# Kernel optimization log

Hardware: AMD Instinct MI355X
Metric: run time of the kernel (lower is better)

The kernel has to match this reference:

```python
import jax, jax.numpy as jnp
import numpy as np
from jax import lax

B, T, IN, H, DIM = 128, 1024, 64, 128, 64


def setup_inputs() -> dict:
    key = jax.random.key(0)
    ks = jax.random.split(key, 14)
    s = 0.05
    return {
        "x": jax.random.normal(ks[0], (B, T, IN), jnp.float32),
        "is_init": jax.random.randint(ks[1], (B, T, 1), 0, 2).astype(bool),
        "hx": jax.random.normal(ks[2], (B, H), jnp.float32),
        # MLP: Linear(IN,128) + ELU, Linear(128,128) + ELU
        "W1": jax.random.normal(ks[3], (128, IN), jnp.float32) * s,
        "b1": jnp.zeros((128,), jnp.float32),
        "W2": jax.random.normal(ks[4], (128, 128), jnp.float32) * s,
        "b2": jnp.zeros((128,), jnp.float32),
        # GRU params (torch layout: [3H, in] with gate order r,z,n)
        "W_ih": jax.random.normal(ks[5], (3 * H, 128), jnp.float32) * s,
        "b_ih": jnp.zeros((3 * H,), jnp.float32),
        "W_hh": jax.random.normal(ks[6], (3 * H, H), jnp.float32) * s,
        "b_hh": jnp.zeros((3 * H,), jnp.float32),
        # output head Linear(128, DIM)
        "W_out": jax.random.normal(ks[7], (DIM, 128), jnp.float32) * s,
        "b_out": jnp.zeros((DIM,), jnp.float32),
    }


def _gru_with_reset(xg, init_mask, h0, W_hh, b_hh):
    # xg: [T,B,3H] precomputed input-side gates; init_mask: [T,B,1] float
    def step(h, inp):
        xg_t, m_t = inp
        h = h * (1.0 - m_t)                       # reset hidden where is_init
        hg = h @ W_hh.T + b_hh                    # [B,3H]
        xr, xz, xn = jnp.split(xg_t, 3, axis=-1)
        hr, hz, hn = jnp.split(hg, 3, axis=-1)
        r = jax.nn.sigmoid(xr + hr)
        z = jax.nn.sigmoid(xz + hz)
        n = jnp.tanh(xn + r * hn)
        h_new = (1.0 - z) * n + z * h
        return h_new, h_new

    hT, ys = lax.scan(step, h0, (xg, init_mask))
    return ys, hT


def reference(x, is_init, hx, W1, b1, W2, b2, W_ih, b_ih, W_hh, b_hh, W_out, b_out):
    # MLP (ELU activations)
    h = jax.nn.elu(x @ W1.T + b1)
    h = jax.nn.elu(h @ W2.T + b2)                 # [B,T,128]
    # precompute input-side gate projections for all timesteps (one big GEMM)
    xg = h @ W_ih.T + b_ih                        # [B,T,3H]
    xg_t = jnp.transpose(xg, (1, 0, 2))           # [T,B,3H]
    m_t = jnp.transpose(is_init.astype(x.dtype), (1, 0, 2))  # [T,B,1]
    ys, hT = _gru_with_reset(xg_t, m_t, hx, W_hh, b_hh)
    y = jnp.transpose(ys, (1, 0, 2))              # [B,T,H]
    out = y @ W_out.T + b_out                     # [B,T,DIM]
    return out, hT
```

## Files before the change

kernel.cpp:

```cpp
#include <hip/hip_runtime.h>


#define T_SZ 1024

typedef __attribute__((ext_vector_type(8))) short short8;
typedef __attribute__((ext_vector_type(4))) float f32x4;
typedef unsigned long long u64;
typedef unsigned int uint32;

__device__ __forceinline__ unsigned short f2b(float f){
  return __builtin_bit_cast(unsigned short, (__bf16)f);
}
__device__ __forceinline__ float b2f(unsigned int hs){
  unsigned int u = hs << 16;
  return __builtin_bit_cast(float, u);
}
__device__ __forceinline__ short8 load_w8(const float* __restrict__ p){
  const float4* q = (const float4*)p;
  float4 u0 = q[0], u1 = q[1];
  short8 v;
  v[0]=(short)f2b(u0.x); v[1]=(short)f2b(u0.y); v[2]=(short)f2b(u0.z); v[3]=(short)f2b(u0.w);
  v[4]=(short)f2b(u1.x); v[5]=(short)f2b(u1.y); v[6]=(short)f2b(u1.z); v[7]=(short)f2b(u1.w);
  return v;
}
__device__ __forceinline__ float elu(float v){ return v > 0.f ? v : __expf(v) - 1.f; }
__device__ __forceinline__ float sigm(float x){ return 1.f / (1.f + __expf(-x)); }
__device__ __forceinline__ float tanh_fast(float x){
  x = fminf(fmaxf(x, -15.f), 15.f);
  float e = __expf(-2.f * x);
  return (1.f - e) / (1.f + e);
}
#define MFMA16(a,b,c) __builtin_amdgcn_mfma_f32_16x16x32_bf16(a, b, c, 0, 0, 0)


__global__ __launch_bounds__(512) void wprep(const float* __restrict__ Whh, uint4* __restrict__ wbf){
  int rec = blockIdx.x*512 + threadIdx.x;
  if(rec >= 6144) return;
  int q  = rec & 3;
  int n_ = (rec >> 2) & 127;
  int ks = (rec >> 9) & 3;
  int gt = rec >> 11;
  const float* p = Whh + (size_t)(n_ + 128*gt)*128 + ks*32 + q*8;
  uint4 o;
  o.x = (uint32)f2b(p[0]) | ((uint32)f2b(p[1]) << 16);
  o.y = (uint32)f2b(p[2]) | ((uint32)f2b(p[3]) << 16);
  o.z = (uint32)f2b(p[4]) | ((uint32)f2b(p[5]) << 16);
  o.w = (uint32)f2b(p[6]) | ((uint32)f2b(p[7]) << 16);
  wbf[rec] = o;
}

__global__ __launch_bounds__(512) void seg_build(const int* __restrict__ ii, uint32* C){
  __shared__ uint32 lh[1024];
  __shared__ uint32 lbase[1024];
  __shared__ uint32 ssum[512];
  __shared__ uint32 sbase;
  uint32* segs = C + 4096;
  const int tid = threadIdx.x;
  const int wv = tid >> 6, lane = tid & 63;
  const int b = blockIdx.x*8 + wv;

  for(int i = tid; i < 1024; i += 512) lh[i] = 0u;
  __syncthreads();

  u64 bal[16], mb[16];
  #pragma unroll
  for(int c=0;c<16;c++){
    int t = c*64 + lane;
    int m = ii[b*T_SZ + t];
    mb[c]  = __ballot(m != 0);
    bal[c] = __ballot((m != 0) || (t == 0));
  }
  int fsA[16]; int nx = T_SZ;
  #pragma unroll
  for(int c=15;c>=0;c--){ fsA[c]=nx; if(bal[c]) nx = c*64 + __builtin_ctzll(bal[c]); }

  int lenA[16], tA[16], rkA[16];
  #pragma unroll
  for(int c=0;c<16;c++){
    lenA[c] = 0;
    if((bal[c] >> lane) & 1ull){
      int t = c*64 + lane;
      u64 hi = (lane < 63) ? (bal[c] >> (lane+1)) : 0ull;
      int nxt = hi ? (t + 1 + __builtin_ctzll(hi)) : fsA[c];
      int len = nxt - t;
      int rst = (int)((mb[c] >> lane) & 1ull);
      len -= rst; t += rst;
      if(len > 0){
        lenA[c] = len; tA[c] = t;
        rkA[c] = (int)atomicAdd(&lh[1024 - len], 1u);
      }
    }
  }
  __syncthreads();

  uint32 c0 = lh[2*tid], c1 = lh[2*tid+1];
  ssum[tid] = c0 + c1;
  __syncthreads();
  #pragma unroll
  for(int off=1; off<512; off<<=1){
    uint32 v = (tid >= off) ? ssum[tid-off] : 0u;
    __syncthreads();
    ssum[tid] += v;
    __syncthreads();
  }
  uint32 excl = tid ? ssum[tid-1] : 0u;
  lbase[2*tid]   = excl;
  lbase[2*tid+1] = excl + c0;
  uint32 total = ssum[511];
  uint32 padded = (total + 15u) & ~15u;
  if(tid == 0){
    sbase = atomicAdd(&C[2], padded);
    atomicAdd(&C[1], padded >> 4);
  }
  __syncthreads();
  const uint32 base = sbase;

  #pragma unroll
  for(int c=0;c<16;c++){
    if(lenA[c] > 0){
      uint32 slot = base + lbase[1024 - lenA[c]] + (uint32)rkA[c];
      segs[slot] = ((uint32)b << 21) | ((uint32)tA[c] << 11) | (uint32)lenA[c];
    }
  }
  for(uint32 i = total + tid; i < padded; i += 512) segs[base + i] = 0u;
}

__global__ __launch_bounds__(512) void fused_mlp(
    const float* __restrict__ x, const int* __restrict__ ii,
    const float* __restrict__ W1, const float* __restrict__ b1,
    const float* __restrict__ W2, const float* __restrict__ b2,
    const float* __restrict__ Wih, const float* __restrict__ bih,
    const float* __restrict__ bhh,
    unsigned short* __restrict__ xg, unsigned short* __restrict__ ys,
    float* __restrict__ hT)
{
  __shared__ __align__(16) char smem[35840];
  unsigned short* xs  = (unsigned short*)smem;
  unsigned short* h1l = (unsigned short*)(smem + 18432);
  unsigned short* h2l = (unsigned short*)smem;
  __shared__ int iil[64];
  const int tid = threadIdx.x;
  const int wv = tid >> 6, l = tid & 63, quad = l >> 4, col = l & 15;
  const int n = 16*wv + col;

  short8 w1f[2], w2f[4], wif[3][4];
  #pragma unroll
  for(int ks=0; ks<2; ks++) w1f[ks] = load_w8(W1 + n*64  + ks*32 + quad*8);
  #pragma unroll
  for(int ks=0; ks<4; ks++) w2f[ks] = load_w8(W2 + n*128 + ks*32 + quad*8);
  #pragma unroll
  for(int gt=0; gt<3; gt++){
    #pragma unroll
    for(int ks=0; ks<4; ks++)
      wif[gt][ks] = load_w8(Wih + (n + 128*gt)*128 + ks*32 + quad*8);
  }
  const float b1v = b1[n], b2v = b2[n];
  float bihv[3], bhhv[3];
  #pragma unroll
  for(int gt=0; gt<3; gt++){ bihv[gt] = bih[n + 128*gt]; bhhv[gt] = bhh[n + 128*gt]; }

  const int srow = tid >> 5, sk = tid & 31;

  for(int tile = blockIdx.x; tile < 2048; tile += gridDim.x){
    const int g = tile & 7, t0 = (tile >> 3) * 4;
    __syncthreads();
    {
      const float* src = x + (size_t)(16*g + srow)*(T_SZ*64) + (size_t)t0*64;
      #pragma unroll
      for(int j=0; j<2; j++){
        int s = sk + 32*j;
        float4 v = ((const float4*)src)[s];
        int tt = s >> 4, k = (s & 15) * 4;
        unsigned short* dst = xs + (tt*16 + srow)*72 + k;
        dst[0]=f2b(v.x); dst[1]=f2b(v.y); dst[2]=f2b(v.z); dst[3]=f2b(v.w);
      }
    }
    if(tid < 64) iil[tid] = ii[(16*g + (tid & 15))*T_SZ + t0 + (tid >> 4)];
    __syncthreads();
    #pragma unroll
    for(int tt=0; tt<4; tt++){
      f32x4 acc = {b1v, b1v, b1v, b1v};
      #pragma unroll
      for(int ks=0; ks<2; ks++){
        short8 a = *(const short8*)&xs[(tt*16 + col)*72 + ks*32 + quad*8];
        acc = MFMA16(a, w1f[ks], acc);
      }
      #pragma unroll
      for(int r=0; r<4; r++)
        h1l[(tt*16 + quad*4 + r)*136 + n] = f2b(elu(acc[r]));
    }
    __syncthreads();
    #pragma unroll
    for(int tt=0; tt<4; tt++){
      f32x4 acc = {b2v, b2v, b2v, b2v};
      #pragma unroll
      for(int ks=0; ks<4; ks++){
        short8 a = *(const short8*)&h1l[(tt*16 + col)*136 + ks*32 + quad*8];
        acc = MFMA16(a, w2f[ks], acc);
      }
      #pragma unroll
      for(int r=0; r<4; r++)
        h2l[(tt*16 + quad*4 + r)*136 + n] = f2b(elu(acc[r]));
    }
    __syncthreads();
    uint32 xgo[4];
    #pragma unroll
    for(int r=0; r<4; r++)
      xgo[r] = (((uint32)(16*g + quad*4 + r) << 10) + (uint32)t0) * 384u + (uint32)n;
    #pragma unroll
    for(int tt=0; tt<4; tt++){
      f32x4 a0 = {bihv[0], bihv[0], bihv[0], bihv[0]};
      f32x4 a1 = {bihv[1], bihv[1], bihv[1], bihv[1]};
      f32x4 a2 = {bihv[2], bihv[2], bihv[2], bihv[2]};
      #pragma unroll
      for(int ks=0; ks<4; ks++){
        short8 a = *(const short8*)&h2l[(tt*16 + col)*136 + ks*32 + quad*8];
        a0 = MFMA16(a, wif[0][ks], a0);
        a1 = MFMA16(a, wif[1][ks], a1);
        a2 = MFMA16(a, wif[2][ks], a2);
      }
      const int t = t0 + tt;
      #pragma unroll
      for(int r=0; r<4; r++){
        int row = quad*4 + r;
        unsigned short* p = xg + xgo[r] + (uint32)(tt*384);
        p[0]   = f2b(a0[r]);
        p[128] = f2b(a1[r]);
        p[256] = f2b(a2[r]);
        if(iil[tt*16 + row] != 0){
          float rr = sigm(a0[r] + bhhv[0]);
          float zz = sigm(a1[r] + bhhv[1]);
          float nn = tanh_fast(a2[r] + rr*bhhv[2]);
          float h1 = (1.f - zz)*nn;
          ys[((size_t)(t*8 + g)*16 + row)*128 + n] = f2b(h1);
          if(t == T_SZ-1)
            hT[(16*g + row)*128 + n] = h1;
        }
      }
    }
  }
}

__global__ __launch_bounds__(512) void gru_seg_scan(
    const unsigned short* __restrict__ xg,
    const float* __restrict__ hx,
    const uint4* __restrict__ wbf, const float* __restrict__ bhh,
    const uint32* __restrict__ C,
    unsigned short* __restrict__ ys, float* __restrict__ hT)
{
  __shared__ unsigned short hl[2][16*136];
  __shared__ unsigned short xbuf[2][16*772];
  __shared__ int srb[16], srt[16], srlen[16];
  const uint32 ntile = C[1];
  const uint32 tile = blockIdx.x;
  if(tile >= ntile) return;

  const int tid = threadIdx.x;
  const int wv = tid >> 6, l = tid & 63, quad = l >> 4, col = l & 15;
  const int nidx = 16*wv + col;
  const int frow = tid >> 5, fk = tid & 31;
  const uint32* segs = C + 4096;

  short8 whf[3][4];
  float bhv[3];
  #pragma unroll
  for(int gt=0; gt<3; gt++){
    bhv[gt] = bhh[nidx + 128*gt];
    #pragma unroll
    for(int ks=0; ks<4; ks++){
      uint4 w = wbf[((gt*4 + ks)*128 + nidx)*4 + quad];
      whf[gt][ks] = __builtin_bit_cast(short8, w);
    }
  }

  if(tid < 16){
    uint32 w = segs[16*tile + (uint32)tid];
    srb[tid] = (int)(w >> 21);
    srt[tid] = (int)((w >> 11) & 1023u);
    srlen[tid] = (int)(w & 2047u);
  }
  __syncthreads();
  const int maxlen = srlen[0];
  const int fb = srb[frow], ft = srt[frow], fl = srlen[frow];

  float hreg[4];
  #pragma unroll
  for(int r=0; r<4; r++){
    int row = quad*4 + r;
    int b = srb[row], t0 = srt[row];
    float h0 = 0.f;
    if(srlen[row] > 0){
      h0 = (t0 == 0) ? hx[b*128 + nidx]
                     : b2f(ys[((size_t)((t0-1)*8 + (b>>4))*16 + (b&15))*128 + nidx]);
    }
    hreg[r] = h0;
    hl[0][row*136 + nidx] = f2b(h0);
  }
  {
    const unsigned short* src = xg + ((size_t)fb*T_SZ + ft)*384;
    unsigned short* xb = &xbuf[0][frow*772];
    #pragma unroll
    for(int i2=0; i2<3; i2++)
      *(u64*)(xb + i2*128 + fk*4) = *(const u64*)(src + i2*128 + fk*4);
  }

  int cur = 0;
  for(int i=0; i<maxlen; i++){
    __syncthreads();
    short8 af[4];
    #pragma unroll
    for(int ks=0; ks<4; ks++)
      af[ks] = *(const short8*)&hl[cur][col*136 + ks*32 + quad*8];
    f32x4 ar = {bhv[0], bhv[0], bhv[0], bhv[0]};
    f32x4 az = {bhv[1], bhv[1], bhv[1], bhv[1]};
    f32x4 an = {bhv[2], bhv[2], bhv[2], bhv[2]};
    #pragma unroll
    for(int ks=0; ks<4; ks++){
      ar = MFMA16(af[ks], whf[0][ks], ar);
      az = MFMA16(af[ks], whf[1][ks], az);
      an = MFMA16(af[ks], whf[2][ks], an);
    }
    u64 p0, p1, p2;
    {
      int tc = (i+1 < fl) ? i+1 : (fl > 0 ? fl-1 : 0);
      const unsigned short* src = xg + ((size_t)fb*T_SZ + (ft + tc))*384;
      p0 = *(const u64*)(src +       fk*4);
      p1 = *(const u64*)(src + 128 + fk*4);
      p2 = *(const u64*)(src + 256 + fk*4);
    }
    if(i >= 1 && i <= fl){
      int t = ft + i - 1;
      u64 hv = *(const u64*)&hl[cur][frow*136 + fk*4];
      *(u64*)(ys + ((size_t)(t*8 + (fb>>4))*16 + (fb&15))*128 + fk*4) = hv;
      if(i == fl && ft + fl == T_SZ){
        #pragma unroll
        for(int j=0; j<4; j++)
          hT[fb*128 + fk*4 + j] = b2f(hl[cur][frow*136 + fk*4 + j]);
      }
    }
    const unsigned short* xb = &xbuf[cur][0];
    #pragma unroll
    for(int r=0; r<4; r++){
      int row = quad*4 + r;
      float xrv = b2f(xb[row*772 +       nidx]);
      float xzv = b2f(xb[row*772 + 128 + nidx]);
      float xnv = b2f(xb[row*772 + 256 + nidx]);
      float rr = sigm(xrv + ar[r]);
      float zz = sigm(xzv + az[r]);
      float nn = tanh_fast(xnv + rr*an[r]);
      float hnew = (1.f - zz)*nn + zz*hreg[r];
      hreg[r] = hnew;
      hl[cur^1][row*136 + nidx] = f2b(hnew);
    }
    {
      unsigned short* xb2 = &xbuf[cur^1][frow*772];
      *(u64*)(xb2 +       fk*4) = p0;
      *(u64*)(xb2 + 128 + fk*4) = p1;
      *(u64*)(xb2 + 256 + fk*4) = p2;
    }
    cur ^= 1;
  }
  __syncthreads();
  if(maxlen >= 1 && fl == maxlen){
    int t = ft + maxlen - 1;
    u64 hv = *(const u64*)&hl[cur][frow*136 + fk*4];
    *(u64*)(ys + ((size_t)(t*8 + (fb>>4))*16 + (fb&15))*128 + fk*4) = hv;
    if(ft + fl == T_SZ){
      #pragma unroll
      for(int j=0; j<4; j++)
        hT[fb*128 + fk*4 + j] = b2f(hl[cur][frow*136 + fk*4 + j]);
    }
  }
}

__global__ __launch_bounds__(256) void out_gemm(
    const unsigned short* __restrict__ ys,
    const float* __restrict__ Wout, const float* __restrict__ bout,
    float* __restrict__ outp)
{
  const int tid = threadIdx.x;
  const int wv = tid >> 6, l = tid & 63, quad = l >> 4, col = l & 15;
  const int n = 16*wv + col;
  short8 wof[4];
  #pragma unroll
  for(int ks=0; ks<4; ks++) wof[ks] = load_w8(Wout + n*128 + ks*32 + quad*8);
  const float bov = bout[n];
  for(int tile = blockIdx.x; tile < 8192; tile += gridDim.x){
    const int t = tile >> 3, g = tile & 7;
    const unsigned short* yt = ys + (size_t)tile * 16 * 128;
    f32x4 acc = {bov, bov, bov, bov};
    #pragma unroll
    for(int ks=0; ks<4; ks++){
      short8 a = *(const short8*)&yt[col*128 + ks*32 + quad*8];
      acc = MFMA16(a, wof[ks], acc);
    }
    #pragma unroll
    for(int r=0; r<4; r++)
      outp[(size_t)(16*g + quad*4 + r)*(T_SZ*64) + (size_t)t*64 + n] = acc[r];
  }
}

extern "C" void kernel_launch(void* const* d_in, const int* in_sizes, int n_in,
                              void* d_out, int out_size, void* d_ws, size_t ws_size,
                              hipStream_t stream)
{
  const float* x    = (const float*)d_in[0];
  const int*   ii   = (const int*)  d_in[1];
  const float* hx   = (const float*)d_in[2];
  const float* W1   = (const float*)d_in[3];
  const float* b1   = (const float*)d_in[4];
  const float* W2   = (const float*)d_in[5];
  const float* b2   = (const float*)d_in[6];
  const float* Wih  = (const float*)d_in[7];
  const float* bih  = (const float*)d_in[8];
  const float* Whh  = (const float*)d_in[9];
  const float* bhh  = (const float*)d_in[10];
  const float* Wout = (const float*)d_in[11];
  const float* bout = (const float*)d_in[12];

  float* outp = (float*)d_out;
  float* hT   = outp + (size_t)128 * T_SZ * 64;
  uint32* C   = (uint32*)d_out;
  uint4* wbf  = (uint4*)((char*)d_out + (1u<<20));

  unsigned short* xg = (unsigned short*)d_ws;
  unsigned short* ys = (unsigned short*)((char*)d_ws + 100663296ull);

  hipMemsetAsync(C, 0, 64, stream);
  wprep      <<<dim3(12),   dim3(512),  0, stream>>>(Whh, wbf);
  seg_build  <<<dim3(16),   dim3(512),  0, stream>>>(ii, C);
  fused_mlp  <<<dim3(512),  dim3(512),  0, stream>>>(x, ii, W1, b1, W2, b2, Wih, bih, bhh, xg, ys, hT);
  gru_seg_scan<<<dim3(4160),dim3(512),  0, stream>>>(xg, hx, wbf, bhh, C, ys, hT);
  out_gemm   <<<dim3(2048), dim3(256),  0, stream>>>(ys, Wout, bout, outp);
}
```

Measured before the change: 256.1 us.

## Software-pipeline fused MLP tiles and use hardware reciprocal in gates

The fused MLP kernel now issues the global loads for the next tile's input and reset mask, then runs the previous tile's input-gate projection while those loads are in flight. Input staging and mask buffers are double-buffered, and the GEMM stage moves to a separate shared buffer so it can overlap the loads. Sigmoid and tanh divisions become hardware reciprocal approximations. This doubles shared memory to about 70KB per block, which may lower occupancy, and the reciprocal slightly reduces precision.

Result: faster. 235.0 us (-8.2%).

```diff
diff --git a/kernel.cpp b/kernel.cpp
--- a/kernel.cpp
+++ b/kernel.cpp
@@ -23,12 +23,13 @@
   v[4]=(short)f2b(u1.x); v[5]=(short)f2b(u1.y); v[6]=(short)f2b(u1.z); v[7]=(short)f2b(u1.w);
   return v;
 }
+__device__ __forceinline__ float rcp_f(float x){ return __builtin_amdgcn_rcpf(x); }
 __device__ __forceinline__ float elu(float v){ return v > 0.f ? v : __expf(v) - 1.f; }
-__device__ __forceinline__ float sigm(float x){ return 1.f / (1.f + __expf(-x)); }
+__device__ __forceinline__ float sigm(float x){ return rcp_f(1.f + __expf(-x)); }
 __device__ __forceinline__ float tanh_fast(float x){
   x = fminf(fmaxf(x, -15.f), 15.f);
   float e = __expf(-2.f * x);
-  return (1.f - e) / (1.f + e);
+  return (1.f - e) * rcp_f(1.f + e);
 }
 #define MFMA16(a,b,c) __builtin_amdgcn_mfma_f32_16x16x32_bf16(a, b, c, 0, 0, 0)
 
@@ -134,11 +135,12 @@
     unsigned short* __restrict__ xg, unsigned short* __restrict__ ys,
     float* __restrict__ hT)
 {
-  __shared__ __align__(16) char smem[35840];
-  unsigned short* xs  = (unsigned short*)smem;
-  unsigned short* h1l = (unsigned short*)(smem + 18432);
-  unsigned short* h2l = (unsigned short*)smem;
-  __shared__ int iil[64];
+  __shared__ __align__(16) char smem[71680];
+  unsigned short* xs0 = (unsigned short*)smem;
+  unsigned short* xs1 = (unsigned short*)(smem + 18432);
+  unsigned short* h1l = (unsigned short*)(smem + 36864);
+  unsigned short* h2l = (unsigned short*)(smem + 54272);
+  __shared__ int iil[2][64];
   const int tid = threadIdx.x;
   const int wv = tid >> 6, l = tid & 63, quad = l >> 4, col = l & 15;
   const int n = 16*wv + col;
@@ -161,52 +163,11 @@
 
   const int srow = tid >> 5, sk = tid & 31;
 
-  for(int tile = blockIdx.x; tile < 2048; tile += gridDim.x){
-    const int g = tile & 7, t0 = (tile >> 3) * 4;
-    __syncthreads();
-    {
-      const float* src = x + (size_t)(16*g + srow)*(T_SZ*64) + (size_t)t0*64;
-      #pragma unroll
-      for(int j=0; j<2; j++){
-        int s = sk + 32*j;
-        float4 v = ((const float4*)src)[s];
-        int tt = s >> 4, k = (s & 15) * 4;
-        unsigned short* dst = xs + (tt*16 + srow)*72 + k;
-        dst[0]=f2b(v.x); dst[1]=f2b(v.y); dst[2]=f2b(v.z); dst[3]=f2b(v.w);
-      }
-    }
-    if(tid < 64) iil[tid] = ii[(16*g + (tid & 15))*T_SZ + t0 + (tid >> 4)];
-    __syncthreads();
-    #pragma unroll
-    for(int tt=0; tt<4; tt++){
-      f32x4 acc = {b1v, b1v, b1v, b1v};
-      #pragma unroll
-      for(int ks=0; ks<2; ks++){
-        short8 a = *(const short8*)&xs[(tt*16 + col)*72 + ks*32 + quad*8];
-        acc = MFMA16(a, w1f[ks], acc);
-      }
-      #pragma unroll
-      for(int r=0; r<4; r++)
-        h1l[(tt*16 + quad*4 + r)*136 + n] = f2b(elu(acc[r]));
-    }
-    __syncthreads();
-    #pragma unroll
-    for(int tt=0; tt<4; tt++){
-      f32x4 acc = {b2v, b2v, b2v, b2v};
-      #pragma unroll
-      for(int ks=0; ks<4; ks++){
-        short8 a = *(const short8*)&h1l[(tt*16 + col)*136 + ks*32 + quad*8];
-        acc = MFMA16(a, w2f[ks], acc);
-      }
-      #pragma unroll
-      for(int r=0; r<4; r++)
-        h2l[(tt*16 + quad*4 + r)*136 + n] = f2b(elu(acc[r]));
-    }
-    __syncthreads();
+  auto stage3 = [&](int g3, int t03, const int* __restrict__ iilp){
     uint32 xgo[4];
     #pragma unroll
     for(int r=0; r<4; r++)
-      xgo[r] = (((uint32)(16*g + quad*4 + r) << 10) + (uint32)t0) * 384u + (uint32)n;
+      xgo[r] = (((uint32)(16*g3 + quad*4 + r) << 10) + (uint32)t03) * 384u + (uint32)n;
     #pragma unroll
     for(int tt=0; tt<4; tt++){
       f32x4 a0 = {bihv[0], bihv[0], bihv[0], bihv[0]};
@@ -219,7 +180,7 @@
         a1 = MFMA16(a, wif[1][ks], a1);
         a2 = MFMA16(a, wif[2][ks], a2);
       }
-      const int t = t0 + tt;
+      const int t = t03 + tt;
       #pragma unroll
       for(int r=0; r<4; r++){
         int row = quad*4 + r;
@@ -227,18 +188,68 @@
         p[0]   = f2b(a0[r]);
         p[128] = f2b(a1[r]);
         p[256] = f2b(a2[r]);
-        if(iil[tt*16 + row] != 0){
+        if(iilp[tt*16 + row] != 0){
           float rr = sigm(a0[r] + bhhv[0]);
           float zz = sigm(a1[r] + bhhv[1]);
           float nn = tanh_fast(a2[r] + rr*bhhv[2]);
           float h1 = (1.f - zz)*nn;
-          ys[((size_t)(t*8 + g)*16 + row)*128 + n] = f2b(h1);
+          ys[((size_t)(t*8 + g3)*16 + row)*128 + n] = f2b(h1);
           if(t == T_SZ-1)
-            hT[(16*g + row)*128 + n] = h1;
+            hT[(16*g3 + row)*128 + n] = h1;
         }
       }
     }
-  }
+  };
+
+  int have_prev = 0, pg = 0, pt0 = 0, p = 0;
+  for(int tile = blockIdx.x; tile < 2048; tile += gridDim.x){
+    const int g = tile & 7, t0 = (tile >> 3) * 4;
+    unsigned short* xs = p ? xs1 : xs0;
+    const float* src = x + (size_t)(16*g + srow)*(T_SZ*64) + (size_t)t0*64;
+    float4 v0 = ((const float4*)src)[sk];
+    float4 v1 = ((const float4*)src)[sk + 32];
+    int iv = 0;
+    if(tid < 64) iv = ii[(16*g + (tid & 15))*T_SZ + t0 + (tid >> 4)];
+    if(have_prev) stage3(pg, pt0, iil[p^1]);
+    {
+      int s0 = sk, tt0 = s0 >> 4, k0 = (s0 & 15)*4;
+      unsigned short* d0 = xs + (tt0*16 + srow)*72 + k0;
+      d0[0]=f2b(v0.x); d0[1]=f2b(v0.y); d0[2]=f2b(v0.z); d0[3]=f2b(v0.w);
+      int s1 = sk + 32, tt1 = s1 >> 4, k1 = (s1 & 15)*4;
+      unsigned short* d1 = xs + (tt1*16 + srow)*72 + k1;
+      d1[0]=f2b(v1.x); d1[1]=f2b(v1.y); d1[2]=f2b(v1.z); d1[3]=f2b(v1.w);
+    }
+    if(tid < 64) iil[p][tid] = iv;
+    __syncthreads();
+    #pragma unroll
+    for(int tt=0; tt<4; tt++){
+      f32x4 acc = {b1v, b1v, b1v, b1v};
+      #pragma unroll
+      for(int ks=0; ks<2; ks++){
+        short8 a = *(const short8*)&xs[(tt*16 + col)*72 + ks*32 + quad*8];
+        acc = MFMA16(a, w1f[ks], acc);
+      }
+      #pragma unroll
+      for(int r=0; r<4; r++)
+        h1l[(tt*16 + quad*4 + r)*136 + n] = f2b(elu(acc[r]));
+    }
+    __syncthreads();
+    #pragma unroll
+    for(int tt=0; tt<4; tt++){
+      f32x4 acc = {b2v, b2v, b2v, b2v};
+      #pragma unroll
+      for(int ks=0; ks<4; ks++){
+        short8 a = *(const short8*)&h1l[(tt*16 + col)*136 + ks*32 + quad*8];
+        acc = MFMA16(a, w2f[ks], acc);
+      }
+      #pragma unroll
+      for(int r=0; r<4; r++)
+        h2l[(tt*16 + quad*4 + r)*136 + n] = f2b(elu(acc[r]));
+    }
+    __syncthreads();
+    have_prev = 1; pg = g; pt0 = t0; p ^= 1;
+  }
+  if(have_prev) stage3(pg, pt0, iil[p^1]);
 }
 
 __global__ __launch_bounds__(512) void gru_seg_scan(
```

## Split fused MLP into separate MLP and gate-projection kernels with prepacked bf16 weights

Applied to the files above, without the earlier changes.

The single fused MLP + input-gate projection kernel becomes two kernels. mlp2 writes the second ELU activation as bf16 into the ys buffer, and xgproj reloads it to compute the xg gates and the reset-step outputs. Weight prep now also packs W1, W2 and W_ih into bf16 MFMA fragment order, so the kernels load ready-made fragments instead of converting fp32 each time. Sigmoid and tanh use a hardware reciprocal instead of a divide. The split lowers per-kernel register pressure and allows larger grids, at the cost of an extra global round trip for the intermediate activations and one more launch.

New measurement: 224.9 us. -12.2%, faster.

```diff
diff --git a/kernel.cpp b/kernel.cpp
--- a/kernel.cpp
+++ b/kernel.cpp
@@ -15,38 +15,46 @@
   unsigned int u = hs << 16;
   return __builtin_bit_cast(float, u);
 }
-__device__ __forceinline__ short8 load_w8(const float* __restrict__ p){
-  const float4* q = (const float4*)p;
-  float4 u0 = q[0], u1 = q[1];
-  short8 v;
-  v[0]=(short)f2b(u0.x); v[1]=(short)f2b(u0.y); v[2]=(short)f2b(u0.z); v[3]=(short)f2b(u0.w);
-  v[4]=(short)f2b(u1.x); v[5]=(short)f2b(u1.y); v[6]=(short)f2b(u1.z); v[7]=(short)f2b(u1.w);
-  return v;
-}
+__device__ __forceinline__ float rcp_f(float x){ return __builtin_amdgcn_rcpf(x); }
 __device__ __forceinline__ float elu(float v){ return v > 0.f ? v : __expf(v) - 1.f; }
-__device__ __forceinline__ float sigm(float x){ return 1.f / (1.f + __expf(-x)); }
+__device__ __forceinline__ float sigm(float x){ return rcp_f(1.f + __expf(-x)); }
 __device__ __forceinline__ float tanh_fast(float x){
   x = fminf(fmaxf(x, -15.f), 15.f);
   float e = __expf(-2.f * x);
-  return (1.f - e) / (1.f + e);
+  return (1.f - e) * rcp_f(1.f + e);
 }
 #define MFMA16(a,b,c) __builtin_amdgcn_mfma_f32_16x16x32_bf16(a, b, c, 0, 0, 0)
 
-
-__global__ __launch_bounds__(512) void wprep(const float* __restrict__ Whh, uint4* __restrict__ wbf){
+__global__ __launch_bounds__(512) void wprep(
+    const float* __restrict__ Whh, const float* __restrict__ W1,
+    const float* __restrict__ W2,  const float* __restrict__ Wih,
+    uint4* __restrict__ wtab)
+{
   int rec = blockIdx.x*512 + threadIdx.x;
-  if(rec >= 6144) return;
-  int q  = rec & 3;
-  int n_ = (rec >> 2) & 127;
-  int ks = (rec >> 9) & 3;
-  int gt = rec >> 11;
-  const float* p = Whh + (size_t)(n_ + 128*gt)*128 + ks*32 + q*8;
+  if(rec >= 15360) return;
+  const float* p;
+  if(rec < 6144){
+    int q = rec & 3, n_ = (rec >> 2) & 127, ks = (rec >> 9) & 3, gt = rec >> 11;
+    p = Whh + (size_t)(n_ + 128*gt)*128 + ks*32 + q*8;
+  } else if(rec < 7168){
+    int r = rec - 6144;
+    int q = r & 3, n_ = (r >> 2) & 127, ks = r >> 9;
+    p = W1 + (size_t)n_*64 + ks*32 + q*8;
+  } else if(rec < 9216){
+    int r = rec - 7168;
+    int q = r & 3, n_ = (r >> 2) & 127, ks = r >> 9;
+    p = W2 + (size_t)n_*128 + ks*32 + q*8;
+  } else {
+    int r = rec - 9216;
+    int q = r & 3, n_ = (r >> 2) & 127, ks = (r >> 9) & 3, gt = r >> 11;
+    p = Wih + (size_t)(n_ + 128*gt)*128 + ks*32 + q*8;
+  }
   uint4 o;
   o.x = (uint32)f2b(p[0]) | ((uint32)f2b(p[1]) << 16);
   o.y = (uint32)f2b(p[2]) | ((uint32)f2b(p[3]) << 16);
   o.z = (uint32)f2b(p[4]) | ((uint32)f2b(p[5]) << 16);
   o.w = (uint32)f2b(p[6]) | ((uint32)f2b(p[7]) << 16);
-  wbf[rec] = o;
+  wtab[rec] = o;
 }
 
 __global__ __launch_bounds__(512) void seg_build(const int* __restrict__ ii, uint32* C){
@@ -125,45 +133,32 @@
   for(uint32 i = total + tid; i < padded; i += 512) segs[base + i] = 0u;
 }
 
-__global__ __launch_bounds__(512) void fused_mlp(
-    const float* __restrict__ x, const int* __restrict__ ii,
-    const float* __restrict__ W1, const float* __restrict__ b1,
-    const float* __restrict__ W2, const float* __restrict__ b2,
-    const float* __restrict__ Wih, const float* __restrict__ bih,
-    const float* __restrict__ bhh,
-    unsigned short* __restrict__ xg, unsigned short* __restrict__ ys,
-    float* __restrict__ hT)
+__global__ __launch_bounds__(512) void mlp2(
+    const float* __restrict__ x,
+    const uint4* __restrict__ wtab,
+    const float* __restrict__ b1, const float* __restrict__ b2,
+    unsigned short* __restrict__ h2)
 {
   __shared__ __align__(16) char smem[35840];
   unsigned short* xs  = (unsigned short*)smem;
   unsigned short* h1l = (unsigned short*)(smem + 18432);
-  unsigned short* h2l = (unsigned short*)smem;
-  __shared__ int iil[64];
   const int tid = threadIdx.x;
   const int wv = tid >> 6, l = tid & 63, quad = l >> 4, col = l & 15;
   const int n = 16*wv + col;
 
-  short8 w1f[2], w2f[4], wif[3][4];
-  #pragma unroll
-  for(int ks=0; ks<2; ks++) w1f[ks] = load_w8(W1 + n*64  + ks*32 + quad*8);
-  #pragma unroll
-  for(int ks=0; ks<4; ks++) w2f[ks] = load_w8(W2 + n*128 + ks*32 + quad*8);
-  #pragma unroll
-  for(int gt=0; gt<3; gt++){
-    #pragma unroll
-    for(int ks=0; ks<4; ks++)
-      wif[gt][ks] = load_w8(Wih + (n + 128*gt)*128 + ks*32 + quad*8);
-  }
+  short8 w1f[2], w2f[4];
+  #pragma unroll
+  for(int ks=0; ks<2; ks++)
+    w1f[ks] = __builtin_bit_cast(short8, wtab[6144 + (ks*128 + n)*4 + quad]);
+  #pragma unroll
+  for(int ks=0; ks<4; ks++)
+    w2f[ks] = __builtin_bit_cast(short8, wtab[7168 + (ks*128 + n)*4 + quad]);
   const float b1v = b1[n], b2v = b2[n];
-  float bihv[3], bhhv[3];
-  #pragma unroll
-  for(int gt=0; gt<3; gt++){ bihv[gt] = bih[n + 128*gt]; bhhv[gt] = bhh[n + 128*gt]; }
 
   const int srow = tid >> 5, sk = tid & 31;
 
   for(int tile = blockIdx.x; tile < 2048; tile += gridDim.x){
     const int g = tile & 7, t0 = (tile >> 3) * 4;
-    __syncthreads();
     {
       const float* src = x + (size_t)(16*g + srow)*(T_SZ*64) + (size_t)t0*64;
       #pragma unroll
@@ -175,7 +170,6 @@
         dst[0]=f2b(v.x); dst[1]=f2b(v.y); dst[2]=f2b(v.z); dst[3]=f2b(v.w);
       }
     }
-    if(tid < 64) iil[tid] = ii[(16*g + (tid & 15))*T_SZ + t0 + (tid >> 4)];
     __syncthreads();
     #pragma unroll
     for(int tt=0; tt<4; tt++){
@@ -198,11 +192,54 @@
         short8 a = *(const short8*)&h1l[(tt*16 + col)*136 + ks*32 + quad*8];
         acc = MFMA16(a, w2f[ks], acc);
       }
-      #pragma unroll
-      for(int r=0; r<4; r++)
-        h2l[(tt*16 + quad*4 + r)*136 + n] = f2b(elu(acc[r]));
-    }
-    __syncthreads();
+      const int t = t0 + tt;
+      #pragma unroll
+      for(int r=0; r<4; r++){
+        int row = quad*4 + r;
+        h2[((size_t)(t*8 + g)*16 + row)*128 + n] = f2b(elu(acc[r]));
+      }
+    }
+  }
+}
+
+__global__ __launch_bounds__(512) void xgproj(
+    const unsigned short* h2, const int* __restrict__ ii,
+    const uint4* __restrict__ wtab,
+    const float* __restrict__ bih, const float* __restrict__ bhh,
+    unsigned short* __restrict__ xg, unsigned short* ys,
+    float* __restrict__ hT)
+{
+  __shared__ __align__(16) unsigned short h2l[4*16*136];
+  __shared__ int iil[64];
+  const int tid = threadIdx.x;
+  const int wv = tid >> 6, l = tid & 63, quad = l >> 4, col = l & 15;
+  const int n = 16*wv + col;
+
+  short8 wif[3][4];
+  #pragma unroll
+  for(int gt=0; gt<3; gt++){
+    #pragma unroll
+    for(int ks=0; ks<4; ks++)
+      wif[gt][ks] = __builtin_bit_cast(short8, wtab[9216 + ((gt*4 + ks)*128 + n)*4 + quad]);
+  }
+  float bihv[3], bhhv[3];
+  #pragma unroll
+  for(int gt=0; gt<3; gt++){ bihv[gt] = bih[n + 128*gt]; bhhv[gt] = bhh[n + 128*gt]; }
+
+  for(int tile = blockIdx.x; tile < 2048; tile += gridDim.x){
+    const int g = tile & 7, t0 = (tile >> 3) * 4;
+    {
+      const int w = tid >> 3, j = tid & 7;
+      const int tt = w >> 4, row = w & 15;
+      const unsigned short* src = h2 + ((size_t)((t0 + tt)*8 + g)*16 + row)*128 + j*16;
+      unsigned short* dst = &h2l[(tt*16 + row)*136 + j*16];
+      #pragma unroll
+      for(int i2=0; i2<4; i2++)
+        *(u64*)(dst + i2*4) = *(const u64*)(src + i2*4);
+    }
+    if(tid < 64) iil[tid] = ii[(16*g + (tid & 15))*T_SZ + t0 + (tid >> 4)];
+    __syncthreads();
+
     uint32 xgo[4];
     #pragma unroll
     for(int r=0; r<4; r++)
@@ -238,6 +275,7 @@
         }
       }
     }
+    __syncthreads();
   }
 }
 
@@ -383,7 +421,15 @@
   const int n = 16*wv + col;
   short8 wof[4];
   #pragma unroll
-  for(int ks=0; ks<4; ks++) wof[ks] = load_w8(Wout + n*128 + ks*32 + quad*8);
+  for(int ks=0; ks<4; ks++){
+    const float* p = Wout + n*128 + ks*32 + quad*8;
+    const float4* q = (const float4*)p;
+    float4 u0 = q[0], u1 = q[1];
+    short8 v;
+    v[0]=(short)f2b(u0.x); v[1]=(short)f2b(u0.y); v[2]=(short)f2b(u0.z); v[3]=(short)f2b(u0.w);
+    v[4]=(short)f2b(u1.x); v[5]=(short)f2b(u1.y); v[6]=(short)f2b(u1.z); v[7]=(short)f2b(u1.w);
+    wof[ks] = v;
+  }
   const float bov = bout[n];
   for(int tile = blockIdx.x; tile < 8192; tile += gridDim.x){
     const int t = tile >> 3, g = tile & 7;
@@ -421,15 +467,16 @@
   float* outp = (float*)d_out;
   float* hT   = outp + (size_t)128 * T_SZ * 64;
   uint32* C   = (uint32*)d_out;
-  uint4* wbf  = (uint4*)((char*)d_out + (1u<<20));
+  uint4* wtab = (uint4*)((char*)d_out + (1u<<20));
 
   unsigned short* xg = (unsigned short*)d_ws;
   unsigned short* ys = (unsigned short*)((char*)d_ws + 100663296ull);
 
   hipMemsetAsync(C, 0, 64, stream);
-  wprep      <<<dim3(12),   dim3(512),  0, stream>>>(Whh, wbf);
+  wprep      <<<dim3(30),   dim3(512),  0, stream>>>(Whh, W1, W2, Wih, wtab);
   seg_build  <<<dim3(16),   dim3(512),  0, stream>>>(ii, C);
-  fused_mlp  <<<dim3(512),  dim3(512),  0, stream>>>(x, ii, W1, b1, W2, b2, Wih, bih, bhh, xg, ys, hT);
-  gru_seg_scan<<<dim3(4160),dim3(512),  0, stream>>>(xg, hx, wbf, bhh, C, ys, hT);
+  mlp2       <<<dim3(2048), dim3(512),  0, stream>>>(x, wtab, b1, b2, ys);
+  xgproj     <<<dim3(2048), dim3(512),  0, stream>>>(ys, ii, wtab, bih, bhh, xg, ys, hT);
+  gru_seg_scan<<<dim3(4160),dim3(512),  0, stream>>>(xg, hx, wtab, bhh, C, ys, hT);
   out_gemm   <<<dim3(2048), dim3(256),  0, stream>>>(ys, Wout, bout, outp);
 }
```
